# Performance work log

Hardware: AMD Instinct MI355X
Metric: run time of the kernel (lower is better)

## Reference

```python
import jax, jax.numpy as jnp
import numpy as np

N = 50000       # number of nodes in the batch
K = 32          # max neighbors (padded)
D = 64          # embed_dim
V = 100000      # number of users (u2e vocab)


def setup_inputs() -> dict:
    key = jax.random.key(0)
    ks = jax.random.split(key, 10)
    nodes = jax.random.randint(ks[0], (N,), 0, V)
    neigh_idx = jax.random.randint(ks[1], (N, K), 0, V)
    counts = jax.random.randint(ks[2], (N,), 1, K + 1)          # ragged lengths, >=1
    neigh_mask = jnp.arange(K)[None, :] < counts[:, None]        # [N,K] bool
    u2e = jax.random.normal(ks[3], (V, D), dtype=jnp.float32) * 0.02
    s1 = 1.0 / np.sqrt(2 * D)
    s2 = 1.0 / np.sqrt(D)
    W1 = jax.random.normal(ks[4], (2 * D, D), dtype=jnp.float32) * s1
    b1 = jnp.zeros((D,), dtype=jnp.float32)
    W2 = jax.random.normal(ks[5], (D, D), dtype=jnp.float32) * s2
    b2 = jnp.zeros((D,), dtype=jnp.float32)
    W3 = jax.random.normal(ks[6], (D, 1), dtype=jnp.float32) * s2
    b3 = jnp.zeros((1,), dtype=jnp.float32)
    return {"u2e": u2e, "W1": W1, "b1": b1, "W2": W2, "b2": b2,
            "W3": W3, "b3": b3, "nodes": nodes, "neigh_idx": neigh_idx,
            "neigh_mask": neigh_mask}


def reference(u2e, W1, b1, W2, b2, W3, b3, nodes, neigh_idx, neigh_mask):
    # Gather neighbor and center-node embeddings (the per-node loop, vectorized)
    e_u = u2e[neigh_idx]                                   # [N,K,D]
    u_rep = u2e[nodes]                                     # [N,D]
    # GraphRec attention MLP on concat([neighbor, center]) -> scalar score
    x = jnp.concatenate(
        [e_u, jnp.broadcast_to(u_rep[:, None, :], e_u.shape)], axis=-1)  # [N,K,2D]
    h = jax.nn.relu(x @ W1 + b1)                           # [N,K,D]
    h = jax.nn.relu(h @ W2 + b2)                           # [N,K,D]
    scores = (h @ W3 + b3)[..., 0]                         # [N,K]
    neg = jnp.asarray(-1e9, dtype=scores.dtype)
    att = jax.nn.softmax(jnp.where(neigh_mask, scores, neg), axis=-1)  # [N,K]
    att = att * neigh_mask.astype(att.dtype)
    # att_history = (e_u^T @ att)^T, per node: weighted neighbor sum
    out = jnp.einsum('nk,nkd->nd', att, e_u)               # [N,D]
    return out
```

## Files before the change

### kernel.cpp

```cpp
#include <hip/hip_runtime.h>
#include <hip/hip_bf16.h>

typedef __bf16 bf16x8 __attribute__((ext_vector_type(8)));
typedef __bf16 bf16x4 __attribute__((ext_vector_type(4)));
typedef float  f32x4  __attribute__((ext_vector_type(4)));

__global__ void detect_mask_kernel(const unsigned* __restrict__ mw, int nwords,
                                   int* __restrict__ flag) {
    int any = 0;
    for (int i = blockIdx.x * blockDim.x + threadIdx.x; i < nwords;
         i += gridDim.x * blockDim.x)
        if (mw[i] > 1u) any = 1;
    if (__any(any)) {
        if ((threadIdx.x & 63) == 0) atomicOr(flag, 1);
    }
}

__global__ __launch_bounds__(256, 3) void graphrec_agg_kernel(
    const float* __restrict__ u2e,
    const float* __restrict__ W1, const float* __restrict__ b1,
    const float* __restrict__ W2, const float* __restrict__ b2,
    const float* __restrict__ W3, const float* __restrict__ b3,
    const int* __restrict__ nodes, const int* __restrict__ neigh_idx,
    const void* __restrict__ mask, const int* __restrict__ flag,
    float* __restrict__ out, int N)
{
    __shared__ __align__(16) __bf16 w1f[16][64][8];
    __shared__ __align__(16) __bf16 tile[4][32][72];
    __shared__ __align__(16) __bf16 urep[4][64];
    __shared__ float att_s[4][32];

    const int tid = threadIdx.x;
    const int w = tid >> 6;
    const int l = tid & 63;
    const int g = l >> 4;
    const int c = l & 15;

    for (int f = w; f < 16; f += 4) {
        int kt = f >> 2, nt = f & 3;
        int r0 = kt * 32 + g * 8, col = nt * 16 + c;
        bf16x8 t;
        #pragma unroll
        for (int i = 0; i < 8; ++i) t[i] = (__bf16)W1[(r0 + i) * 64 + col];
        *(bf16x8*)&w1f[f][l][0] = t;
    }
    __syncthreads();

    bf16x8 w2r[8];
    #pragma unroll
    for (int f = 0; f < 8; ++f) {
        int kt = f >> 2, nt = f & 3;
        int r0 = kt * 32 + g * 8, col = nt * 16 + c;
        #pragma unroll
        for (int i = 0; i < 8; ++i) w2r[f][i] = (__bf16)W2[(r0 + i) * 64 + col];
    }

    float b1v[4], b2v[4], w3v[4];
    #pragma unroll
    for (int nt = 0; nt < 4; ++nt) {
        b1v[nt] = b1[nt * 16 + c];
        b2v[nt] = b2[nt * 16 + c];
        w3v[nt] = W3[nt * 16 + c];
    }
    const float b3s = b3[0];
    const int layout8 = *flag;
    const unsigned char* m8p  = (const unsigned char*)mask;
    const int*           m32p = (const int*)mask;

    const int stride = gridDim.x * 4;
    int nA = blockIdx.x * 4 + w;
    int nB = nA + stride;

    int vidxA = 0, unA = 0; bool mvA = false;
    if (nA < N) {
        if (l < 32) {
            int o = nA * 32 + l;
            vidxA = neigh_idx[o];
            mvA = layout8 ? (m8p[o] != 0) : (m32p[o] != 0);
        }
        unA = nodes[nA];
    }
    int vidxB = 0, unB = 0; bool mvB = false;
    if (nB < N) {
        if (l < 32) {
            int o = nB * 32 + l;
            vidxB = neigh_idx[o];
            mvB = layout8 ? (m8p[o] != 0) : (m32p[o] != 0);
        }
        unB = nodes[nB];
    }

    f32x4 rr[8]; float urv = 0.f;
    if (nA < N) {
        #pragma unroll
        for (int kb = 0; kb < 8; ++kb) {
            int idx = __shfl(vidxA, kb * 4 + g);
            rr[kb] = *(const f32x4*)(u2e + (size_t)idx * 64 + c * 4);
        }
        urv = u2e[(size_t)unA * 64 + l];
    }

    for (; nA < N; nA += stride, nB += stride) {
        int nC = nB + stride;
        int vidxC = 0, unC = 0; bool mvC = false;
        if (nC < N) {
            if (l < 32) {
                int o = nC * 32 + l;
                vidxC = neigh_idx[o];
                mvC = layout8 ? (m8p[o] != 0) : (m32p[o] != 0);
            }
            unC = nodes[nC];
        }

        unsigned long long bal = __ballot(mvA);
        urep[w][l] = (__bf16)urv;
        #pragma unroll
        for (int kb = 0; kb < 8; ++kb) {
            int k = kb * 4 + g;
            bf16x4 bv;
            bv[0] = (__bf16)rr[kb][0]; bv[1] = (__bf16)rr[kb][1];
            bv[2] = (__bf16)rr[kb][2]; bv[3] = (__bf16)rr[kb][3];
            *(bf16x4*)&tile[w][k][c * 4] = bv;
        }

        f32x4 rn[8]; float urvn;
        #pragma unroll
        for (int kb = 0; kb < 8; ++kb) {
            int idx = __shfl(vidxB, kb * 4 + g);
            rn[kb] = *(const f32x4*)(u2e + (size_t)idx * 64 + c * 4);
        }
        urvn = u2e[(size_t)unB * 64 + l];

        bf16x8 a2 = *(const bf16x8*)&urep[w][g * 8];
        bf16x8 a3 = *(const bf16x8*)&urep[w][32 + g * 8];
        #pragma unroll
        for (int mt = 0; mt < 2; ++mt) {
            const __bf16* arow = &tile[w][mt * 16 + c][0];
            bf16x8 a0 = *(const bf16x8*)(arow + g * 8);
            bf16x8 a1 = *(const bf16x8*)(arow + 32 + g * 8);
            #pragma unroll
            for (int nt = 0; nt < 4; ++nt) {
                f32x4 cc = {0.f, 0.f, 0.f, 0.f};
                cc = __builtin_amdgcn_mfma_f32_16x16x32_bf16(a0, *(const bf16x8*)&w1f[0 + nt][l][0], cc, 0, 0, 0);
                cc = __builtin_amdgcn_mfma_f32_16x16x32_bf16(a1, *(const bf16x8*)&w1f[4 + nt][l][0], cc, 0, 0, 0);
                cc = __builtin_amdgcn_mfma_f32_16x16x32_bf16(a2, *(const bf16x8*)&w1f[8 + nt][l][0], cc, 0, 0, 0);
                cc = __builtin_amdgcn_mfma_f32_16x16x32_bf16(a3, *(const bf16x8*)&w1f[12 + nt][l][0], cc, 0, 0, 0);
                #pragma unroll
                for (int r = 0; r < 4; ++r) {
                    float hv = fmaxf(cc[r] + b1v[nt], 0.f);
                    tile[w][mt * 16 + g * 4 + r][nt * 16 + c] = (__bf16)hv;
                }
            }
        }

        float p[2][4];
        #pragma unroll
        for (int mt = 0; mt < 2; ++mt) {
            const __bf16* arow = &tile[w][mt * 16 + c][0];
            bf16x8 a0 = *(const bf16x8*)(arow + g * 8);
            bf16x8 a1 = *(const bf16x8*)(arow + 32 + g * 8);
            float pr0 = 0.f, pr1 = 0.f, pr2 = 0.f, pr3 = 0.f;
            #pragma unroll
            for (int nt = 0; nt < 4; ++nt) {
                f32x4 cc = {0.f, 0.f, 0.f, 0.f};
                cc = __builtin_amdgcn_mfma_f32_16x16x32_bf16(a0, w2r[0 + nt], cc, 0, 0, 0);
                cc = __builtin_amdgcn_mfma_f32_16x16x32_bf16(a1, w2r[4 + nt], cc, 0, 0, 0);
                pr0 += fmaxf(cc[0] + b2v[nt], 0.f) * w3v[nt];
                pr1 += fmaxf(cc[1] + b2v[nt], 0.f) * w3v[nt];
                pr2 += fmaxf(cc[2] + b2v[nt], 0.f) * w3v[nt];
                pr3 += fmaxf(cc[3] + b2v[nt], 0.f) * w3v[nt];
            }
            p[mt][0] = pr0; p[mt][1] = pr1; p[mt][2] = pr2; p[mt][3] = pr3;
        }

        float s[8];
        #pragma unroll
        for (int m = 0; m < 8; ++m) {
            float v = p[m >> 2][m & 3];
            v += __shfl_xor(v, 1);
            v += __shfl_xor(v, 2);
            v += __shfl_xor(v, 4);
            v += __shfl_xor(v, 8);
            s[m] = v + b3s;
        }

        bool vald[8];
        float m8 = -1e30f;
        #pragma unroll
        for (int m = 0; m < 8; ++m) {
            int k = (m >> 2) * 16 + g * 4 + (m & 3);
            vald[m] = ((bal >> k) & 1ull) != 0;
            if (vald[m]) m8 = fmaxf(m8, s[m]);
        }
        m8 = fmaxf(m8, __shfl_xor(m8, 16));
        m8 = fmaxf(m8, __shfl_xor(m8, 32));
        float es[8], ls = 0.f;
        #pragma unroll
        for (int m = 0; m < 8; ++m) {
            es[m] = vald[m] ? __expf(s[m] - m8) : 0.f;
            ls += es[m];
        }
        ls += __shfl_xor(ls, 16);
        ls += __shfl_xor(ls, 32);
        float inv = (ls > 0.f) ? 1.f / ls : 0.f;
        if (c == 0) {
            #pragma unroll
            for (int m = 0; m < 8; ++m) {
                int k = (m >> 2) * 16 + g * 4 + (m & 3);
                att_s[w][k] = es[m] * inv;
            }
        }

        float o0 = 0.f, o1 = 0.f, o2 = 0.f, o3 = 0.f;
        #pragma unroll
        for (int kb = 0; kb < 8; ++kb) {
            float a = att_s[w][kb * 4 + g];
            o0 += a * rr[kb][0]; o1 += a * rr[kb][1];
            o2 += a * rr[kb][2]; o3 += a * rr[kb][3];
        }
        o0 += __shfl_xor(o0, 16); o0 += __shfl_xor(o0, 32);
        o1 += __shfl_xor(o1, 16); o1 += __shfl_xor(o1, 32);
        o2 += __shfl_xor(o2, 16); o2 += __shfl_xor(o2, 32);
        o3 += __shfl_xor(o3, 16); o3 += __shfl_xor(o3, 32);
        if (g == 0) {
            f32x4 ov = {o0, o1, o2, o3};
            *(f32x4*)(out + (size_t)nA * 64 + c * 4) = ov;
        }

        #pragma unroll
        for (int kb = 0; kb < 8; ++kb) rr[kb] = rn[kb];
        urv = urvn;
        mvA = mvB;
        vidxB = vidxC; mvB = mvC; unB = unC;
    }
}

extern "C" void kernel_launch(void* const* d_in, const int* in_sizes, int n_in,
                              void* d_out, int out_size, void* d_ws, size_t ws_size,
                              hipStream_t stream) {
    const float* u2e = (const float*)d_in[0];
    const float* W1  = (const float*)d_in[1];
    const float* b1  = (const float*)d_in[2];
    const float* W2  = (const float*)d_in[3];
    const float* b2  = (const float*)d_in[4];
    const float* W3  = (const float*)d_in[5];
    const float* b3  = (const float*)d_in[6];
    const int* nodes     = (const int*)d_in[7];
    const int* neigh_idx = (const int*)d_in[8];
    const void* mask     = d_in[9];

    const int N = in_sizes[7];
    int* flag = (int*)d_ws;

    hipMemsetAsync(flag, 0, sizeof(int), stream);
    int nwords = in_sizes[9] / 4;
    detect_mask_kernel<<<128, 256, 0, stream>>>((const unsigned*)mask, nwords, flag);

    graphrec_agg_kernel<<<768, 256, 0, stream>>>(
        u2e, W1, b1, W2, b2, W3, b3, nodes, neigh_idx, mask, flag,
        (float*)d_out, N);
}
```

Measured before the change: 234.1 us.

## Gather neighbor embeddings from a bf16 copy of the embedding table

Adds a pre-pass that converts the full u2e table to bf16 in workspace, then gathers 16-byte bf16 rows in the main kernel, halving the bytes of the random-access gather. The weighted output sum now uses bf16-rounded embeddings instead of fp32 ones, which reduces accuracy. The center-node vector is broadcast by lane shuffles instead of a shared-memory buffer, and launch bounds and grid size are raised for more occupancy. The conversion pass reads and writes the whole table on every call, which adds its own cost.

```diff
diff --git a/kernel.cpp b/kernel.cpp
--- a/kernel.cpp
+++ b/kernel.cpp
@@ -4,6 +4,7 @@
 typedef __bf16 bf16x8 __attribute__((ext_vector_type(8)));
 typedef __bf16 bf16x4 __attribute__((ext_vector_type(4)));
 typedef float  f32x4  __attribute__((ext_vector_type(4)));
+typedef short  short8 __attribute__((ext_vector_type(8)));
 
 __global__ void detect_mask_kernel(const unsigned* __restrict__ mw, int nwords,
                                    int* __restrict__ flag) {
@@ -16,8 +17,24 @@
     }
 }
 
-__global__ __launch_bounds__(256, 3) void graphrec_agg_kernel(
-    const float* __restrict__ u2e,
+__global__ void cvt_bf16_kernel(const float* __restrict__ src,
+                                __bf16* __restrict__ dst, int n) {
+    for (int i = (blockIdx.x * blockDim.x + threadIdx.x) * 8; i < n;
+         i += gridDim.x * blockDim.x * 8) {
+        f32x4 a = *(const f32x4*)(src + i);
+        f32x4 b = *(const f32x4*)(src + i + 4);
+        bf16x8 o;
+        o[0] = (__bf16)a[0]; o[1] = (__bf16)a[1];
+        o[2] = (__bf16)a[2]; o[3] = (__bf16)a[3];
+        o[4] = (__bf16)b[0]; o[5] = (__bf16)b[1];
+        o[6] = (__bf16)b[2]; o[7] = (__bf16)b[3];
+        *(bf16x8*)(dst + i) = o;
+    }
+}
+
+template <int BF16SRC>
+__global__ __launch_bounds__(256, 4) void graphrec_agg_kernel(
+    const float* __restrict__ u2e, const __bf16* __restrict__ tbl,
     const float* __restrict__ W1, const float* __restrict__ b1,
     const float* __restrict__ W2, const float* __restrict__ b2,
     const float* __restrict__ W3, const float* __restrict__ b3,
@@ -27,14 +44,14 @@
 {
     __shared__ __align__(16) __bf16 w1f[16][64][8];
     __shared__ __align__(16) __bf16 tile[4][32][72];
-    __shared__ __align__(16) __bf16 urep[4][64];
     __shared__ float att_s[4][32];
-
     const int tid = threadIdx.x;
     const int w = tid >> 6;
     const int l = tid & 63;
     const int g = l >> 4;
     const int c = l & 15;
+    const int j = l >> 3;
+    const int m = l & 7;
 
     for (int f = w; f < 16; f += 4) {
         int kt = f >> 2, nt = f & 3;
@@ -66,6 +83,7 @@
     const int layout8 = *flag;
     const unsigned char* m8p  = (const unsigned char*)mask;
     const int*           m32p = (const int*)mask;
+    const unsigned short* t16 = (const unsigned short*)tbl;
 
     const int stride = gridDim.x * 4;
     int nA = blockIdx.x * 4 + w;
@@ -90,14 +108,26 @@
         unB = nodes[nB];
     }
 
-    f32x4 rr[8]; float urv = 0.f;
+    bf16x8 rr16[4];
+    f32x4  rrf[8];
+    bf16x4 rbf[8];
+    int urvi = 0; float urvf = 0.f;
     if (nA < N) {
-        #pragma unroll
-        for (int kb = 0; kb < 8; ++kb) {
-            int idx = __shfl(vidxA, kb * 4 + g);
-            rr[kb] = *(const f32x4*)(u2e + (size_t)idx * 64 + c * 4);
-        }
-        urv = u2e[(size_t)unA * 64 + l];
+        if (BF16SRC) {
+            #pragma unroll
+            for (int it = 0; it < 4; ++it) {
+                int idx = __shfl(vidxA, it * 8 + j);
+                rr16[it] = *(const bf16x8*)(tbl + (size_t)idx * 64 + m * 8);
+            }
+            urvi = t16[(size_t)unA * 64 + l];
+        } else {
+            #pragma unroll
+            for (int kb = 0; kb < 8; ++kb) {
+                int idx = __shfl(vidxA, kb * 4 + g);
+                rrf[kb] = *(const f32x4*)(u2e + (size_t)idx * 64 + c * 4);
+            }
+            urvf = u2e[(size_t)unA * 64 + l];
+        }
     }
 
     for (; nA < N; nA += stride, nB += stride) {
@@ -112,27 +142,58 @@
             unC = nodes[nC];
         }
 
+        bf16x8 rn16[4]; f32x4 rnf[8];
+        int urvin = 0; float urvfn = 0.f;
+        if (BF16SRC) {
+            #pragma unroll
+            for (int it = 0; it < 4; ++it) {
+                int idx = __shfl(vidxB, it * 8 + j);
+                rn16[it] = *(const bf16x8*)(tbl + (size_t)idx * 64 + m * 8);
+            }
+            urvin = t16[(size_t)unB * 64 + l];
+        } else {
+            #pragma unroll
+            for (int kb = 0; kb < 8; ++kb) {
+                int idx = __shfl(vidxB, kb * 4 + g);
+                rnf[kb] = *(const f32x4*)(u2e + (size_t)idx * 64 + c * 4);
+            }
+            urvfn = u2e[(size_t)unB * 64 + l];
+        }
+
         unsigned long long bal = __ballot(mvA);
-        urep[w][l] = (__bf16)urv;
-        #pragma unroll
-        for (int kb = 0; kb < 8; ++kb) {
-            int k = kb * 4 + g;
-            bf16x4 bv;
-            bv[0] = (__bf16)rr[kb][0]; bv[1] = (__bf16)rr[kb][1];
-            bv[2] = (__bf16)rr[kb][2]; bv[3] = (__bf16)rr[kb][3];
-            *(bf16x4*)&tile[w][k][c * 4] = bv;
-        }
-
-        f32x4 rn[8]; float urvn;
-        #pragma unroll
-        for (int kb = 0; kb < 8; ++kb) {
-            int idx = __shfl(vidxB, kb * 4 + g);
-            rn[kb] = *(const f32x4*)(u2e + (size_t)idx * 64 + c * 4);
-        }
-        urvn = u2e[(size_t)unB * 64 + l];
-
-        bf16x8 a2 = *(const bf16x8*)&urep[w][g * 8];
-        bf16x8 a3 = *(const bf16x8*)&urep[w][32 + g * 8];
+        if (BF16SRC) {
+            #pragma unroll
+            for (int it = 0; it < 4; ++it)
+                *(bf16x8*)&tile[w][it * 8 + j][m * 8] = rr16[it];
+        } else {
+            #pragma unroll
+            for (int kb = 0; kb < 8; ++kb) {
+                bf16x4 bv;
+                bv[0] = (__bf16)rrf[kb][0]; bv[1] = (__bf16)rrf[kb][1];
+                bv[2] = (__bf16)rrf[kb][2]; bv[3] = (__bf16)rrf[kb][3];
+                *(bf16x4*)&tile[w][kb * 4 + g][c * 4] = bv;
+                rbf[kb] = bv;
+            }
+        }
+
+        bf16x8 a2, a3;
+        if (BF16SRC) {
+            short8 t2, t3;
+            #pragma unroll
+            for (int i = 0; i < 8; ++i) {
+                t2[i] = (short)__shfl(urvi, g * 8 + i);
+                t3[i] = (short)__shfl(urvi, 32 + g * 8 + i);
+            }
+            a2 = __builtin_bit_cast(bf16x8, t2);
+            a3 = __builtin_bit_cast(bf16x8, t3);
+        } else {
+            #pragma unroll
+            for (int i = 0; i < 8; ++i) {
+                a2[i] = (__bf16)__shfl(urvf, g * 8 + i);
+                a3[i] = (__bf16)__shfl(urvf, 32 + g * 8 + i);
+            }
+        }
+
         #pragma unroll
         for (int mt = 0; mt < 2; ++mt) {
             const __bf16* arow = &tile[w][mt * 16 + c][0];
@@ -175,61 +236,92 @@
 
         float s[8];
         #pragma unroll
-        for (int m = 0; m < 8; ++m) {
-            float v = p[m >> 2][m & 3];
+        for (int q = 0; q < 8; ++q) {
+            float v = p[q >> 2][q & 3];
             v += __shfl_xor(v, 1);
             v += __shfl_xor(v, 2);
             v += __shfl_xor(v, 4);
             v += __shfl_xor(v, 8);
-            s[m] = v + b3s;
+            s[q] = v + b3s;
         }
 
         bool vald[8];
-        float m8 = -1e30f;
-        #pragma unroll
-        for (int m = 0; m < 8; ++m) {
-            int k = (m >> 2) * 16 + g * 4 + (m & 3);
-            vald[m] = ((bal >> k) & 1ull) != 0;
-            if (vald[m]) m8 = fmaxf(m8, s[m]);
-        }
-        m8 = fmaxf(m8, __shfl_xor(m8, 16));
-        m8 = fmaxf(m8, __shfl_xor(m8, 32));
+        float mx = -1e30f;
+        #pragma unroll
+        for (int q = 0; q < 8; ++q) {
+            int k = (q >> 2) * 16 + g * 4 + (q & 3);
+            vald[q] = ((bal >> k) & 1ull) != 0;
+            if (vald[q]) mx = fmaxf(mx, s[q]);
+        }
+        mx = fmaxf(mx, __shfl_xor(mx, 16));
+        mx = fmaxf(mx, __shfl_xor(mx, 32));
         float es[8], ls = 0.f;
         #pragma unroll
-        for (int m = 0; m < 8; ++m) {
-            es[m] = vald[m] ? __expf(s[m] - m8) : 0.f;
-            ls += es[m];
+        for (int q = 0; q < 8; ++q) {
+            es[q] = vald[q] ? __expf(s[q] - mx) : 0.f;
+            ls += es[q];
         }
         ls += __shfl_xor(ls, 16);
         ls += __shfl_xor(ls, 32);
         float inv = (ls > 0.f) ? 1.f / ls : 0.f;
         if (c == 0) {
             #pragma unroll
-            for (int m = 0; m < 8; ++m) {
-                int k = (m >> 2) * 16 + g * 4 + (m & 3);
-                att_s[w][k] = es[m] * inv;
-            }
-        }
-
-        float o0 = 0.f, o1 = 0.f, o2 = 0.f, o3 = 0.f;
-        #pragma unroll
-        for (int kb = 0; kb < 8; ++kb) {
-            float a = att_s[w][kb * 4 + g];
-            o0 += a * rr[kb][0]; o1 += a * rr[kb][1];
-            o2 += a * rr[kb][2]; o3 += a * rr[kb][3];
-        }
-        o0 += __shfl_xor(o0, 16); o0 += __shfl_xor(o0, 32);
-        o1 += __shfl_xor(o1, 16); o1 += __shfl_xor(o1, 32);
-        o2 += __shfl_xor(o2, 16); o2 += __shfl_xor(o2, 32);
-        o3 += __shfl_xor(o3, 16); o3 += __shfl_xor(o3, 32);
-        if (g == 0) {
-            f32x4 ov = {o0, o1, o2, o3};
-            *(f32x4*)(out + (size_t)nA * 64 + c * 4) = ov;
-        }
-
-        #pragma unroll
-        for (int kb = 0; kb < 8; ++kb) rr[kb] = rn[kb];
-        urv = urvn;
+            for (int q = 0; q < 8; ++q) {
+                int k = (q >> 2) * 16 + g * 4 + (q & 3);
+                att_s[w][k] = es[q] * inv;
+            }
+        }
+
+        if (BF16SRC) {
+            float o[8];
+            #pragma unroll
+            for (int d = 0; d < 8; ++d) o[d] = 0.f;
+            #pragma unroll
+            for (int it = 0; it < 4; ++it) {
+                float a = att_s[w][it * 8 + j];
+                #pragma unroll
+                for (int d = 0; d < 8; ++d) o[d] += a * (float)rr16[it][d];
+            }
+            #pragma unroll
+            for (int d = 0; d < 8; ++d) {
+                o[d] += __shfl_xor(o[d], 8);
+                o[d] += __shfl_xor(o[d], 16);
+                o[d] += __shfl_xor(o[d], 32);
+            }
+            if (j == 0) {
+                f32x4 ov = {o[0], o[1], o[2], o[3]};
+                *(f32x4*)(out + (size_t)nA * 64 + m * 8) = ov;
+            } else if (j == 1) {
+                f32x4 ov = {o[4], o[5], o[6], o[7]};
+                *(f32x4*)(out + (size_t)nA * 64 + m * 8 + 4) = ov;
+            }
+        } else {
+            float o0 = 0.f, o1 = 0.f, o2 = 0.f, o3 = 0.f;
+            #pragma unroll
+            for (int kb = 0; kb < 8; ++kb) {
+                float a = att_s[w][kb * 4 + g];
+                o0 += a * (float)rbf[kb][0]; o1 += a * (float)rbf[kb][1];
+                o2 += a * (float)rbf[kb][2]; o3 += a * (float)rbf[kb][3];
+            }
+            o0 += __shfl_xor(o0, 16); o0 += __shfl_xor(o0, 32);
+            o1 += __shfl_xor(o1, 16); o1 += __shfl_xor(o1, 32);
+            o2 += __shfl_xor(o2, 16); o2 += __shfl_xor(o2, 32);
+            o3 += __shfl_xor(o3, 16); o3 += __shfl_xor(o3, 32);
+            if (g == 0) {
+                f32x4 ov = {o0, o1, o2, o3};
+                *(f32x4*)(out + (size_t)nA * 64 + c * 4) = ov;
+            }
+        }
+
+        if (BF16SRC) {
+            #pragma unroll
+            for (int it = 0; it < 4; ++it) rr16[it] = rn16[it];
+            urvi = urvin;
+        } else {
+            #pragma unroll
+            for (int kb = 0; kb < 8; ++kb) rrf[kb] = rnf[kb];
+            urvf = urvfn;
+        }
         mvA = mvB;
         vidxB = vidxC; mvB = mvC; unB = unC;
     }
@@ -249,14 +341,26 @@
     const int* neigh_idx = (const int*)d_in[8];
     const void* mask     = d_in[9];
 
-    const int N = in_sizes[7];
+    const int N  = in_sizes[7];
+    const int VD = in_sizes[0];
+
     int* flag = (int*)d_ws;
+    __bf16* tbl = (__bf16*)((char*)d_ws + 256);
+    const size_t needed = 256 + (size_t)VD * sizeof(__bf16);
+    const bool use16 = (ws_size >= needed);
 
     hipMemsetAsync(flag, 0, sizeof(int), stream);
     int nwords = in_sizes[9] / 4;
     detect_mask_kernel<<<128, 256, 0, stream>>>((const unsigned*)mask, nwords, flag);
 
-    graphrec_agg_kernel<<<768, 256, 0, stream>>>(
-        u2e, W1, b1, W2, b2, W3, b3, nodes, neigh_idx, mask, flag,
-        (float*)d_out, N);
+    if (use16) {
+        cvt_bf16_kernel<<<2048, 256, 0, stream>>>(u2e, tbl, VD);
+        graphrec_agg_kernel<1><<<1536, 256, 0, stream>>>(
+            u2e, tbl, W1, b1, W2, b2, W3, b3, nodes, neigh_idx, mask, flag,
+            (float*)d_out, N);
+    } else {
+        graphrec_agg_kernel<0><<<1536, 256, 0, stream>>>(
+            u2e, (const __bf16*)u2e, W1, b1, W2, b2, W3, b3, nodes, neigh_idx,
+            mask, flag, (float*)d_out, N);
+    }
 }
```

Measured after the change: 389.5 us. 1.66x slower.
